# Kernel tuning notes

Hardware: AMD Instinct MI355X
Metric: run time of the kernel (lower is better)

Reference implementation:

```python
import jax, jax.numpy as jnp
import numpy as np

T = 3              # num_ntype (slots)
NH = 64            # num_hidden == num_classes
HEADS = (4, 4, 1)
NUM_ETYPES = 5
EDGE_DIM = 64
N_NODES = 20000
NEG_SLOPE = 0.2
ALPHA = 0.05       # residual-attention blend
EPS = 1e-12


def _l2_by_slot(x):
    # l2_norm with l2BySlot='True': normalize each ntype slot independently
    n = x.shape[0]
    xs = x.reshape(n, T, -1)
    nrm = jnp.linalg.norm(xs, axis=2, keepdims=True)
    return (xs / jnp.maximum(nrm, EPS)).reshape(n, -1)


def _edge_softmax(logits, dst, n):
    # softmax over incoming edges of each destination node
    m = jax.lax.stop_gradient(jax.ops.segment_max(logits, dst, num_segments=n))
    e = jnp.exp(logits - m[dst])
    s = jax.ops.segment_sum(e, dst, num_segments=n)
    return e / s[dst]


def _conv(x, src, dst, etype, W, al, ar, ee_tab, We, ae, res_attn, act):
    # slotGATConv: x [N,T,C], W [T,C,H*O], al/ar [H,T*O], ee_tab [R,De], We [De,H*De], ae [H,De]
    n = x.shape[0]
    H = al.shape[0]
    proj = jnp.einsum('ntc,tcd->ntd', x, W)                     # [N,T,H*O]
    O = proj.shape[-1] // H
    feat = proj.reshape(n, T, H, O).transpose(0, 2, 1, 3).reshape(n, H, T * O)
    el = jnp.einsum('nhd,hd->nh', feat, al)
    er = jnp.einsum('nhd,hd->nh', feat, ar)
    De = ee_tab.shape[1]
    ep = (ee_tab[etype] @ We).reshape(-1, H, De)                # [E,H,De]
    ee = jnp.einsum('ehd,hd->eh', ep, ae)                       # [E,H]
    logit = jax.nn.leaky_relu(el[src] + er[dst] + ee, NEG_SLOPE)
    a = _edge_softmax(logit, dst, n)                            # [E,H]
    if res_attn is not None:
        a = a * (1.0 - ALPHA) + res_attn * ALPHA
    out = jax.ops.segment_sum(feat[src] * a[:, :, None], dst, num_segments=n)  # [N,H,T*O]
    if act:
        out = jax.nn.elu(out)
    return out, a


def _forward(feat0, feat1, feat2, w_in0, b_in0, w_in1, b_in1, w_in2, b_in2,
             l0_W, l0_al, l0_ar, l0_ee, l0_we, l0_ae,
             l1_W, l1_al, l1_ar, l1_ee, l1_we, l1_ae,
             l2_W, l2_al, l2_ar, l2_ee, l2_we, l2_ae,
             dm_W, e_feat, src, dst, left, right, mid):
    feats = [feat0, feat1, feat2]
    lins = [(w_in0, b_in0), (w_in1, b_in1), (w_in2, b_in2)]
    blocks = []
    for t, (f, (w, b)) in enumerate(zip(feats, lins)):
        ft = f @ w + b                                          # [n_t, NH]
        pad = jnp.zeros((f.shape[0], T * NH), ft.dtype)
        blocks.append(pad.at[:, t * NH:(t + 1) * NH].set(ft))   # slot zero-padding
    h = jnp.concatenate(blocks, 0)                              # [N, T*NH]
    emb = [_l2_by_slot(h)]                                      # aggregator='None' -> identity
    x = h.reshape(-1, T, NH)
    out0, a0 = _conv(x, src, dst, e_feat, l0_W, l0_al, l0_ar, l0_ee, l0_we, l0_ae, None, True)
    emb.append(_l2_by_slot(out0.mean(1)))
    x = out0.reshape(-1, HEADS[0], T, NH).transpose(0, 2, 1, 3).reshape(-1, T, HEADS[0] * NH)
    out1, a1 = _conv(x, src, dst, e_feat, l1_W, l1_al, l1_ar, l1_ee, l1_we, l1_ae, a0, True)
    emb.append(_l2_by_slot(out1.mean(1)))
    x = out1.reshape(-1, HEADS[1], T, NH).transpose(0, 2, 1, 3).reshape(-1, T, HEADS[1] * NH)
    out2, _ = _conv(x, src, dst, e_feat, l2_W, l2_al, l2_ar, l2_ee, l2_we, l2_ae, a1, False)
    emb.append(_l2_by_slot(out2.mean(1)))
    # aggregator='None' + inProcessEmb='True': concat per-slot along feature dim
    embs = [e.reshape(-1, T, NH) for e in emb]
    o = jnp.concatenate(embs, 2).reshape(-1, T * NH * len(embs))  # [N, 768]
    le, re = o[left], o[right]
    scores = jnp.zeros(left.shape[0], o.dtype)
    for r in range(NUM_ETYPES):                                 # DistMult per relation
        s = ((le @ dm_W[r]) * re).sum(1)
        scores = jnp.where(mid == r, s, scores)
    return jax.nn.sigmoid(scores)


def setup_inputs() -> dict:
    key = jax.random.key(0)
    ks = iter(jax.random.split(key, 64))
    def nrm(shape, std):
        return jax.random.normal(next(ks), shape, jnp.float32) * std
    counts = [8000, 6000, 6000]
    in_dims = [256, 128, 64]
    inp = {}
    for t in range(T):
        inp[f'feat{t}'] = jax.random.normal(next(ks), (counts[t], in_dims[t]), jnp.float32)
        inp[f'w_in{t}'] = nrm((in_dims[t], NH), 0.1)
        inp[f'b_in{t}'] = nrm((NH,), 0.1)
    Cs = [NH, HEADS[0] * NH, HEADS[1] * NH]
    for l in range(3):
        H = HEADS[l]
        inp[f'l{l}_W'] = nrm((T, Cs[l], H * NH), 0.1)
        inp[f'l{l}_al'] = nrm((H, T * NH), 0.1)
        inp[f'l{l}_ar'] = nrm((H, T * NH), 0.1)
        inp[f'l{l}_ee'] = nrm((NUM_ETYPES, EDGE_DIM), 0.1)
        inp[f'l{l}_we'] = nrm((EDGE_DIM, H * EDGE_DIM), 0.1)
        inp[f'l{l}_ae'] = nrm((H, EDGE_DIM), 0.1)
    D = T * NH * 4
    inp['dm_W'] = nrm((NUM_ETYPES, D, D), 0.05)
    E, L = 200000, 10000
    inp['e_feat'] = jax.random.randint(next(ks), (E,), 0, NUM_ETYPES)
    inp['src'] = jax.random.randint(next(ks), (E,), 0, N_NODES)
    inp['dst'] = jax.random.randint(next(ks), (E,), 0, N_NODES)
    inp['left'] = jax.random.randint(next(ks), (L,), 0, N_NODES)
    inp['right'] = jax.random.randint(next(ks), (L,), 0, N_NODES)
    inp['mid'] = jax.random.randint(next(ks), (L,), 0, NUM_ETYPES)
    return inp


def reference(feat0, feat1, feat2, w_in0, b_in0, w_in1, b_in1, w_in2, b_in2,
              l0_W, l0_al, l0_ar, l0_ee, l0_we, l0_ae,
              l1_W, l1_al, l1_ar, l1_ee, l1_we, l1_ae,
              l2_W, l2_al, l2_ar, l2_ee, l2_we, l2_ae,
              dm_W, e_feat, src, dst, left, right, mid):
    return _forward(feat0, feat1, feat2, w_in0, b_in0, w_in1, b_in1, w_in2, b_in2,
                    l0_W, l0_al, l0_ar, l0_ee, l0_we, l0_ae,
                    l1_W, l1_al, l1_ar, l1_ee, l1_we, l1_ae,
                    l2_W, l2_al, l2_ar, l2_ee, l2_we, l2_ae,
                    dm_W, e_feat, src, dst, left, right, mid)
```

## Files before the change

### kernel.cpp

```cpp
#include <hip/hip_runtime.h>
#include <math.h>

#define N_NODES 20000
#define NPAD    20096
#define N_EDGES 200000
#define N_PAIRS 10000
#define PAIR_PAD 10368
#define DM_TILES 162
#define NBLK    79

typedef __attribute__((ext_vector_type(8))) short s16x8;
typedef __attribute__((ext_vector_type(4))) float f32x4;

__device__ inline float wave_max(float v){
  for (int o = 32; o > 0; o >>= 1) v = fmaxf(v, __shfl_xor(v, o));
  return v;
}
__device__ inline float wave_sum(float v){
  for (int o = 32; o > 0; o >>= 1) v += __shfl_xor(v, o);
  return v;
}
__device__ inline float half_max(float v){
  for (int o = 16; o > 0; o >>= 1) v = fmaxf(v, __shfl_xor(v, o));
  return v;
}
__device__ inline float half_sum(float v){
  for (int o = 16; o > 0; o >>= 1) v += __shfl_xor(v, o);
  return v;
}
__device__ inline short f2bf(float x){
  union { float f; unsigned u; } v; v.f = x;
  unsigned r = (v.u + 0x7FFFu + ((v.u >> 16) & 1u)) >> 16;
  return (short)r;
}
__device__ inline float bf2f(short s){
  union { unsigned u; float f; } v; v.u = ((unsigned)(unsigned short)s) << 16;
  return v.f;
}
__device__ inline int ntype(int s){ return (s < 8000) ? 0 : ((s < 14000) ? 1 : 2); }
__device__ inline float elu1(float x){ return (x > 0.f) ? x : expm1f(x); }

#define OS(i, c) ((i) * 100 + (c))

__global__ void build_h(const float* __restrict__ f0, const float* __restrict__ w0, const float* __restrict__ b0,
                        const float* __restrict__ f1, const float* __restrict__ w1, const float* __restrict__ b1,
                        const float* __restrict__ f2, const float* __restrict__ w2, const float* __restrict__ b2,
                        short* __restrict__ Xb0, short* __restrict__ o_b,
                        int* __restrict__ cnt3, int* __restrict__ cnt5, int* __restrict__ pos5,
                        float* __restrict__ score, int* __restrict__ pairs,
                        float* __restrict__ eall, short* __restrict__ Xb12,
                        short* __restrict__ featb){
  const int blk = blockIdx.x, lane = threadIdx.x;
  const int gid = blk * 64 + lane;
  if (gid < 80000) cnt3[gid] = 0;
  if (gid < 5){ cnt5[gid * 16] = 0; pos5[gid * 16] = 0; }
  if (gid < 10016) score[gid] = 0.f;
  if (gid < PAIR_PAD) pairs[gid] = -1;
  for (int i = gid; i < 480000; i += 160000) eall[i] = 0.f;
  s16x8 z = {};
  if (gid < 4608){
    int t = (gid * 16) / 24576, off = (gid * 16) % 24576;
    short* p = Xb12 + ((size_t)(t * NPAD + N_NODES)) * 256 + off;
    *(s16x8*)p = z; *(s16x8*)(p + 8) = z;
  }
  if (gid < 1152){
    int t = (gid * 16) / 6144, off = (gid * 16) % 6144;
    short* p = Xb0 + ((size_t)(t * NPAD + N_NODES)) * 64 + off;
    *(s16x8*)p = z; *(s16x8*)(p + 8) = z;
  }
  int t, C, nbase; const float *f, *w, *b;
  if (blk < 1000)       { t = 0; nbase = 0;     C = 256; f = f0; w = w0; b = b0; }
  else if (blk < 1750)  { t = 1; nbase = 8000;  C = 128; f = f1; w = w1; b = b1; }
  else                  { t = 2; nbase = 14000; C = 64;  f = f2; w = w2; b = b2; }
  const int n0 = blk * 8;
  const int n0l = n0 - nbase;
  __shared__ float xs[8 * 256];
  const float* fr = f + (size_t)n0l * C;
  for (int i = lane; i < 8 * C; i += 64) xs[i] = fr[i];
  __syncthreads();
  float acc[8];
#pragma unroll
  for (int j = 0; j < 8; j++) acc[j] = b[lane];
  for (int c = 0; c < C; c++){
    float wv = w[c * 64 + lane];
#pragma unroll
    for (int j = 0; j < 8; j++) acc[j] += xs[j * C + c] * wv;
  }
  for (int j = 0; j < 8; j++){
    int n = n0 + j;
    {
      int h = lane >> 4, si = (lane >> 3) & 1, j8 = lane & 7;
      int s0 = (t == 0) ? 1 : 0;
      int s1 = (t == 2) ? 1 : 2;
      int toff = si ? s1 : s0;
      *(s16x8*)(featb + ((size_t)n * 4 + h) * 192 + toff * 64 + j8 * 8) = z;
    }
    for (int tt = 0; tt < 3; tt++)
      Xb0[((size_t)(tt * NPAD) + n) * 64 + lane] = f2bf((tt == t) ? acc[j] : 0.f);
    float ss = wave_sum(acc[j] * acc[j]);
    float sc = 1.f / fmaxf(sqrtf(ss), 1e-12f);
    for (int tt = 0; tt < 3; tt++)
      o_b[(size_t)n * 768 + tt * 256 + lane] = f2bf((tt == t) ? acc[j] * sc : 0.f);
  }
}

__global__ void count_prep_k(const int* __restrict__ dst, const int* __restrict__ srcv,
                             int* __restrict__ cnt3,
                             const int* __restrict__ mid, int* __restrict__ cnt5,
                             const float* __restrict__ lW0, const float* __restrict__ lW1,
                             const float* __restrict__ lW2, const float* __restrict__ dmW,
                             short* __restrict__ Wt0, short* __restrict__ Wt1,
                             short* __restrict__ Wt2, short* __restrict__ Mt,
                             const float* __restrict__ ee0, const float* __restrict__ we0, const float* __restrict__ ae0,
                             const float* __restrict__ ee1, const float* __restrict__ we1, const float* __restrict__ ae1,
                             const float* __restrict__ ee2, const float* __restrict__ we2, const float* __restrict__ ae2,
                             float* __restrict__ ee5f){
  if (blockIdx.x < 782){
    int e = blockIdx.x * 256 + threadIdx.x;
    int lane = threadIdx.x & 63;
    if (e < N_EDGES){
      int tt = ntype(srcv[e]);
      atomicAdd(&cnt3[dst[e] * 4 + tt], 1);
    }
    int r_mine = (e < N_PAIRS) ? mid[e] : -1;
#pragma unroll
    for (int r = 0; r < 5; r++){
      unsigned long long mask = __ballot(r_mine == r);
      if (mask){
        int leader = __ffsll((long long)mask) - 1;
        if (lane == leader) atomicAdd(&cnt5[r * 16], __popcll(mask));
      }
    }
    return;
  }
  int lin = blockIdx.x - 782;
  int z = lin / 576;
  int rem = lin % 576;
  int by = rem / 24, bx = rem % 24;
  if (z == 10){
    int r = bx, L = by;
    if (r >= 5 || L >= 3) return;
    int H = (L == 2) ? 1 : 4;
    const float* eetab = (L == 0) ? ee0 : ((L == 1) ? ee1 : ee2);
    const float* We    = (L == 0) ? we0 : ((L == 1) ? we1 : we2);
    const float* ae    = (L == 0) ? ae0 : ((L == 1) ? ae1 : ae2);
    int h = threadIdx.x >> 6, lane = threadIdx.x & 63;
    if (h >= H) return;
    float v = 0.f;
    for (int k = 0; k < 64; k++) v += eetab[r * 64 + k] * We[k * H * 64 + h * 64 + lane];
    v *= ae[h * 64 + lane];
    v = wave_sum(v);
    if (lane == 0) ee5f[L * 32 + r * H + h] = v;
    return;
  }
  const float* s; short* d; int R, Cc, r0, c0;
  if (z < 5){
    s = dmW + (size_t)z * 589824; d = Mt + (size_t)z * 589824;
    R = 768; Cc = 768; r0 = bx * 32; c0 = by * 32;
  } else if (z < 8){
    if (bx >= 8 || by >= 8) return;
    int t = z - 5;
    s = lW1 + (size_t)t * 65536; d = Wt1 + (size_t)t * 65536;
    R = 256; Cc = 256; r0 = bx * 32; c0 = by * 32;
  } else if (z == 8){
    if (bx >= 6 || by >= 8) return;
    int t = bx >> 1;
    s = lW0 + (size_t)t * 16384; d = Wt0 + (size_t)t * 16384;
    R = 64; Cc = 256; r0 = (bx & 1) * 32; c0 = by * 32;
  } else {
    if (bx >= 8 || by >= 6) return;
    int t = by >> 1;
    s = lW2 + (size_t)t * 16384; d = Wt2 + (size_t)t * 16384;
    R = 256; Cc = 64; r0 = bx * 32; c0 = (by & 1) * 32;
  }
  __shared__ float tile[32][33];
  int tx = threadIdx.x & 31, ty = threadIdx.x >> 5;
  for (int i = 0; i < 32; i += 8){
    int r = r0 + ty + i;
    tile[ty + i][tx] = (r < R && c0 + tx < Cc) ? s[(size_t)r * Cc + c0 + tx] : 0.f;
  }
  __syncthreads();
  for (int i = 0; i < 32; i += 8){
    int c = c0 + ty + i;
    if (c < Cc && r0 + tx < R)
      d[(size_t)c * R + r0 + tx] = f2bf(tile[tx][ty + i]);
  }
}

__global__ void scan1_k(const int* __restrict__ cnt3, int* __restrict__ loc, int* __restrict__ bsum){
  __shared__ int s[256];
  int tid = threadIdx.x;
  int idx = blockIdx.x * 256 + tid;
  int v = (idx < N_NODES) ? (cnt3[idx * 4] + cnt3[idx * 4 + 1] + cnt3[idx * 4 + 2]) : 0;
  s[tid] = v;
  __syncthreads();
  for (int o = 1; o < 256; o <<= 1){
    int u = (tid >= o) ? s[tid - o] : 0;
    __syncthreads();
    s[tid] += u;
    __syncthreads();
  }
  if (idx < N_NODES) loc[idx] = s[tid] - v;
  if (tid == 255) bsum[blockIdx.x] = s[255];
}

__global__ void scan2_k(const int* __restrict__ bsum, int* __restrict__ bofs,
                        const int* __restrict__ cnt5, int* __restrict__ off5){
  __shared__ int s[128];
  int tid = threadIdx.x;
  int v = (tid < NBLK) ? bsum[tid] : 0;
  s[tid] = v;
  __syncthreads();
  for (int o = 1; o < 128; o <<= 1){
    int u = (tid >= o) ? s[tid - o] : 0;
    __syncthreads();
    s[tid] += u;
    __syncthreads();
  }
  if (tid < NBLK) bofs[tid] = s[tid] - v;
  if (tid == 0){
    int r0 = 0;
    for (int r = 0; r < 5; r++){ off5[r] = r0; r0 += ((cnt5[r * 16] + 63) >> 6) << 6; }
  }
}

__global__ void scan3_k(const int* __restrict__ loc, const int* __restrict__ bofs,
                        int* __restrict__ coff, int* __restrict__ cpos,
                        const int* __restrict__ cnt3){
  int idx = blockIdx.x * 256 + threadIdx.x;
  if (idx < N_NODES){
    int v = loc[idx] + bofs[blockIdx.x];
    coff[idx] = v;
    int c0 = cnt3[idx * 4], c1 = cnt3[idx * 4 + 1];
    cpos[idx * 4]     = v;
    cpos[idx * 4 + 1] = v + c0;
    cpos[idx * 4 + 2] = v + c0 + c1;
  }
  if (idx == 0) coff[N_NODES] = N_EDGES;
}

__global__ void scatter_k(const int* __restrict__ dst, const int* __restrict__ srcv,
                          const int* __restrict__ efeat, int* __restrict__ cpos,
                          int* __restrict__ src_sorted, int* __restrict__ et_sorted,
                          const int* __restrict__ mid, const int* __restrict__ off5,
                          int* __restrict__ pos5, int* __restrict__ pairs){
  int e = blockIdx.x * 256 + threadIdx.x;
  int lane = threadIdx.x & 63;
  if (e < N_EDGES){
    int s = srcv[e];
    int tt = ntype(s);
    int p = atomicAdd(&cpos[dst[e] * 4 + tt], 1);
    src_sorted[p] = s;
    et_sorted[p] = efeat[e];
  }
  int r_mine = (e < N_PAIRS) ? mid[e] : -1;
#pragma unroll
  for (int r = 0; r < 5; r++){
    unsigned long long mask = __ballot(r_mine == r);
    if (mask){
      int cnt = __popcll(mask);
      int leader = __ffsll((long long)mask) - 1;
      int base = 0;
      if (lane == leader) base = atomicAdd(&pos5[r * 16], cnt);
      base = __shfl(base, leader);
      if (r_mine == r){
        int rank = __popcll(mask & ((1ull << lane) - 1ull));
        pairs[off5[r] + base + rank] = e;
      }
    }
  }
}

template<int C, int NO, int TYPED>
__global__ void mfma_proj(const short* __restrict__ Xb, const short* __restrict__ Wt,
                          short* __restrict__ featb, const float* __restrict__ al,
                          const float* __restrict__ ar, float* __restrict__ elf,
                          float* __restrict__ erf){
  constexpr int H = NO / 64;
  const int ct = blockIdx.y;
  const int t  = blockIdx.z;
  int tile = blockIdx.x;
  if (TYPED){
    const int lo[3] = {0, 62, 109};
    const int hi[3] = {63, 110, 157};
    tile += lo[t];
    if (tile >= hi[t]) return;
  }
  const int n0 = tile * 128;
  const int tid = threadIdx.x;
  const int w = tid >> 6, lane = tid & 63;
  const int quad = lane >> 4, ln = lane & 15;
  __shared__ __attribute__((aligned(16))) short A_s[128 * 32];
  __shared__ __attribute__((aligned(16))) short B_s[64 * 32];
  const short* Xt  = Xb + (size_t)t * NPAD * C;
  const short* Wtt = Wt + ((size_t)t * NO + ct * 64) * C;
  f32x4 acc[2][4] = {};
  for (int kk = 0; kk < C; kk += 32){
    {
      int row = tid >> 1, half = tid & 1;
      const s16x8* g = (const s16x8*)(Xt + (size_t)(n0 + row) * C + kk + half * 16);
      s16x8 v0 = g[0], v1 = g[1];
      *(s16x8*)(A_s + row * 32 + half * 16) = v0;
      *(s16x8*)(A_s + row * 32 + half * 16 + 8) = v1;
    }
    {
      int row = tid >> 2, chunk = tid & 3;
      s16x8 v = *(const s16x8*)(Wtt + (size_t)row * C + kk + chunk * 8);
      *(s16x8*)(B_s + row * 32 + chunk * 8) = v;
    }
    __syncthreads();
    s16x8 af0 = *(s16x8*)(A_s + (w * 32 + ln) * 32 + quad * 8);
    s16x8 af1 = *(s16x8*)(A_s + (w * 32 + 16 + ln) * 32 + quad * 8);
    s16x8 bf[4];
#pragma unroll
    for (int b = 0; b < 4; b++) bf[b] = *(s16x8*)(B_s + (b * 16 + ln) * 32 + quad * 8);
#pragma unroll
    for (int b = 0; b < 4; b++){
      acc[0][b] = __builtin_amdgcn_mfma_f32_16x16x32_bf16(af0, bf[b], acc[0][b], 0, 0, 0);
      acc[1][b] = __builtin_amdgcn_mfma_f32_16x16x32_bf16(af1, bf[b], acc[1][b], 0, 0, 0);
    }
    __syncthreads();
  }
#pragma unroll
  for (int ar_ = 0; ar_ < 2; ar_++){
#pragma unroll
    for (int i = 0; i < 4; i++){
      int n = n0 + w * 32 + ar_ * 16 + quad * 4 + i;
      if (n >= N_NODES) continue;
#pragma unroll
      for (int b = 0; b < 4; b++){
        int jj = b * 16 + ln;
        featb[((size_t)n * H + ct) * 192 + t * 64 + jj] = f2bf(acc[ar_][b][i]);
      }
    }
  }
  float alv[4], arv[4];
#pragma unroll
  for (int b = 0; b < 4; b++){
    alv[b] = al[ct * 192 + t * 64 + b * 16 + ln];
    arv[b] = ar[ct * 192 + t * 64 + b * 16 + ln];
  }
#pragma unroll
  for (int ar_ = 0; ar_ < 2; ar_++){
#pragma unroll
    for (int i = 0; i < 4; i++){
      float pe = 0.f, pr = 0.f;
#pragma unroll
      for (int b = 0; b < 4; b++){
        pe += acc[ar_][b][i] * alv[b];
        pr += acc[ar_][b][i] * arv[b];
      }
#pragma unroll
      for (int o = 1; o < 16; o <<= 1){
        pe += __shfl_xor(pe, o);
        pr += __shfl_xor(pr, o);
      }
      int n = n0 + w * 32 + ar_ * 16 + quad * 4 + i;
      if (ln == 0 && n < N_NODES){
        atomicAdd(&elf[n * H + ct], pe);
        atomicAdd(&erf[n * H + ct], pr);
      }
    }
  }
}

template<int H, int MODE, int ACT, int TYPED>
__global__ __launch_bounds__(256) void gat_fused(
    const int* __restrict__ csr_off, const int* __restrict__ src_sorted,
    const int* __restrict__ et_sorted,
    const float* __restrict__ el, const float* __restrict__ er, const float* __restrict__ ee5,
    const float* __restrict__ aprev, float* __restrict__ aout,
    const short* __restrict__ featb, short* __restrict__ outb,
    short* __restrict__ o_b, const int* __restrict__ cnt3, int kslice){
  const int wid = threadIdx.x >> 6, lane = threadIdx.x & 63;
  const int half = lane >> 5, hl = lane & 31;
  const int l32 = half << 5;
  const int n0 = blockIdx.x * 8 + wid * 2;
  const int nme = n0 + half;
  __shared__ float a_s[4][64][H];
  __shared__ int   src_s[4][64];
  __shared__ float out_s[4][2][800];
  const char* fb = (const char*)featb;

  const int offm = csr_off[nme];
  const int cntm = csr_off[nme + 1] - offm;
  const int cnto = __shfl_xor(cntm, 32);
  const bool paired = (cntm <= 32) && (cnto <= 32);

  if (paired){
    float ern[H];
    if constexpr (H == 4){
      f32x4 ev = *(const f32x4*)(er + nme * 4);
#pragma unroll
      for (int h = 0; h < 4; h++) ern[h] = ev[h];
    } else ern[0] = er[nme];
    const int p = offm + hl;
    const bool valid = hl < cntm;
    int sidx = 0, r = 0;
    if (valid){ sidx = src_sorted[p]; r = et_sorted[p]; }
    int s0 = __shfl(sidx, l32);
    src_s[wid][lane] = (valid ? sidx : s0) * (H * 384);
    float lg[H];
#pragma unroll
    for (int h = 0; h < H; h++) lg[h] = -1e30f;
    if (valid){
      if constexpr (H == 4){
        f32x4 elv = *(const f32x4*)(el + sidx * 4);
        f32x4 eev = *(const f32x4*)(ee5 + r * 4);
#pragma unroll
        for (int h = 0; h < 4; h++){
          float v = elv[h] + ern[h] + eev[h];
          lg[h] = (v >= 0.f) ? v : 0.2f * v;
        }
      } else {
        float v = el[sidx] + ern[0] + ee5[r];
        lg[0] = (v >= 0.f) ? v : 0.2f * v;
      }
    }
    float ap[4] = {};
    if (MODE > 0 && valid){
      f32x4 av4 = *(const f32x4*)(aprev + (size_t)p * 4);
#pragma unroll
      for (int q = 0; q < 4; q++) ap[q] = av4[q];
    }
    float av[H];
#pragma unroll
    for (int h = 0; h < H; h++){
      float mh = half_max(lg[h]);
      float ex = valid ? __expf(lg[h] - mh) : 0.f;
      float sh = half_sum(ex);
      float a = ex / sh;
      if (MODE == 1) a = 0.95f * a + 0.05f * ap[h];
      if (MODE == 2) a = 0.95f * a + 0.0125f * (ap[0] + ap[1] + ap[2] + ap[3]);
      av[h] = a;
      a_s[wid][lane][h] = valid ? a : 0.f;
    }
    if constexpr (MODE != 2){
      if (valid){
        f32x4 o = {av[0], av[1], av[2], av[3]};
        *(f32x4*)(aout + (size_t)p * 4) = o;
      }
    }

    if constexpr (TYPED && H == 4){
      const int hh = hl >> 3, j8 = hl & 7;
      float acc[3][8] = {};
      const int b1 = cnt3[nme * 4], b2 = b1 + cnt3[nme * 4 + 1];
      const int rb[4] = {0, b1, b2, cntm};
#pragma unroll
      for (int t = 0; t < 3; t++){
        const int sub = hh * 384 + t * 128 + j8 * 16;
        for (int b = rb[t]; b < rb[t + 1]; b += 2){
          int e0 = l32 + b;
          bool v1 = (b + 1) < rb[t + 1];
          int e1 = v1 ? e0 + 1 : e0;
          float a0 = a_s[wid][e0][hh];
          float a1 = v1 ? a_s[wid][e1][hh] : 0.f;
          int so0 = src_s[wid][e0], so1 = src_s[wid][e1];
          s16x8 f0 = *(const s16x8*)(fb + so0 + sub);
          s16x8 f1 = *(const s16x8*)(fb + so1 + sub);
#pragma unroll
          for (int i = 0; i < 8; i++) acc[t][i] += a0 * bf2f(f0[i]) + a1 * bf2f(f1[i]);
        }
      }
#pragma unroll
      for (int t = 0; t < 3; t++){
#pragma unroll
        for (int i = 0; i < 8; i++){
          float v = acc[t][i];
          if (ACT) v = elu1(v);
          out_s[wid][half][OS(i, hh * 24 + t * 8 + j8)] = v;
        }
      }
    } else if constexpr (H == 4){
      const int p0 = hl, p1 = hl + 32, p2 = hl + 64;
      const int h0 = p0 / 24, h1 = p1 / 24, h2 = p2 / 24;
      float acc0[8] = {}, acc1[8] = {}, acc2[8] = {};
      const int cnt2 = (cntm + 1) & ~1;
      for (int b = 0; b < cnt2; b += 2){
        int e0 = l32 + b, e1 = l32 + b + 1;
        int so0 = src_s[wid][e0], so1 = src_s[wid][e1];
        float a00 = a_s[wid][e0][h0], a01 = a_s[wid][e0][h1], a02 = a_s[wid][e0][h2];
        float a10 = a_s[wid][e1][h0], a11 = a_s[wid][e1][h1], a12 = a_s[wid][e1][h2];
        s16x8 f00 = *(const s16x8*)(fb + so0 + p0 * 16);
        s16x8 f01 = *(const s16x8*)(fb + so0 + p1 * 16);
        s16x8 f02 = *(const s16x8*)(fb + so0 + p2 * 16);
        s16x8 f10 = *(const s16x8*)(fb + so1 + p0 * 16);
        s16x8 f11 = *(const s16x8*)(fb + so1 + p1 * 16);
        s16x8 f12 = *(const s16x8*)(fb + so1 + p2 * 16);
#pragma unroll
        for (int i = 0; i < 8; i++){
          acc0[i] += a00 * bf2f(f00[i]) + a10 * bf2f(f10[i]);
          acc1[i] += a01 * bf2f(f01[i]) + a11 * bf2f(f11[i]);
          acc2[i] += a02 * bf2f(f02[i]) + a12 * bf2f(f12[i]);
        }
      }
#pragma unroll
      for (int i = 0; i < 8; i++){
        float v0 = acc0[i], v1 = acc1[i], v2 = acc2[i];
        if (ACT){ v0 = elu1(v0); v1 = elu1(v1); v2 = elu1(v2); }
        out_s[wid][half][OS(i, p0)] = v0;
        out_s[wid][half][OS(i, p1)] = v1;
        out_s[wid][half][OS(i, p2)] = v2;
      }
    } else {
      const int e4 = hl >> 3, cb = hl & 7;
      float acc[3][8] = {};
      for (int b = 0; b < cntm; b += 4){
        int e = l32 + b + e4;
        float a = a_s[wid][e][0];
        int so = src_s[wid][e];
#pragma unroll
        for (int c = 0; c < 3; c++){
          s16x8 fv = *(const s16x8*)(fb + so + (cb * 3 + c) * 16);
#pragma unroll
          for (int i = 0; i < 8; i++) acc[c][i] += a * bf2f(fv[i]);
        }
      }
#pragma unroll
      for (int c = 0; c < 3; c++){
#pragma unroll
        for (int i = 0; i < 8; i++){
          float v = acc[c][i];
          v += __shfl_xor(v, 8); v += __shfl_xor(v, 16);
          if (ACT) v = elu1(v);
          if (e4 == 0) out_s[wid][half][OS(i, cb * 3 + c)] = v;
        }
      }
    }
  } else {
    for (int k = 0; k < 2; k++){
      const int n = n0 + k;
      const int off = csr_off[n];
      const int cnt = csr_off[n + 1] - off;
      float* osk = out_s[wid][k];
      float ern[H];
#pragma unroll
      for (int h = 0; h < H; h++) ern[h] = er[n * H + h];
      if (cnt <= 64){
        int p = off + lane;
        int sidx = 0, r = 0;
        if (lane < cnt){ sidx = src_sorted[p]; r = et_sorted[p]; }
        int src0 = __shfl(sidx, 0);
        src_s[wid][lane] = ((lane < cnt) ? sidx : src0) * (H * 384);
        float lg[H];
#pragma unroll
        for (int h = 0; h < H; h++) lg[h] = -1e30f;
        if (lane < cnt){
#pragma unroll
          for (int h = 0; h < H; h++){
            float v = el[sidx * H + h] + ern[h] + ee5[r * H + h];
            lg[h] = (v >= 0.f) ? v : 0.2f * v;
          }
        }
        float ap[4] = {};
        if (MODE > 0 && lane < cnt){
#pragma unroll
          for (int q = 0; q < 4; q++) ap[q] = aprev[(size_t)p * 4 + q];
        }
        float av[H];
#pragma unroll
        for (int h = 0; h < H; h++){
          float mh = wave_max(lg[h]);
          float ex = (lane < cnt) ? __expf(lg[h] - mh) : 0.f;
          float sh = wave_sum(ex);
          float a = ex / sh;
          if (MODE == 1) a = 0.95f * a + 0.05f * ap[h];
          if (MODE == 2) a = 0.95f * a + 0.0125f * (ap[0] + ap[1] + ap[2] + ap[3]);
          av[h] = a;
          a_s[wid][lane][h] = (lane < cnt) ? a : 0.f;
        }
        if constexpr (MODE != 2){
          if (lane < cnt){
            f32x4 o = {av[0], av[1], av[2], av[3]};
            *(f32x4*)(aout + (size_t)p * 4) = o;
          }
        }
        if constexpr (H == 4){
          const int p0 = lane;
          const int p1 = (lane < 32) ? lane + 64 : lane - 32;
          const int p2 = lane + 32;
          const int hA = p0 / 24, hB = p1 / 24, hC = p2 / 24;
          const int eo2 = lane >> 5;
          float acc0[8] = {}, acc1[8] = {}, acc2[8] = {};
          const int cnt4 = (cnt + 3) & ~3;
          for (int b = 0; b < cnt4; b += 4){
            int eB0 = b + eo2, eB1 = b + 2 + eo2;
            int oA0 = src_s[wid][b],     oB0 = src_s[wid][eB0], oC0 = src_s[wid][b + 1];
            int oA1 = src_s[wid][b + 2], oB1 = src_s[wid][eB1], oC1 = src_s[wid][b + 3];
            float aA0 = a_s[wid][b][hA],     aB0 = a_s[wid][eB0][hB], aC0 = a_s[wid][b + 1][hC];
            float aA1 = a_s[wid][b + 2][hA], aB1 = a_s[wid][eB1][hB], aC1 = a_s[wid][b + 3][hC];
            s16x8 fA0 = *(const s16x8*)(fb + oA0 + p0 * 16);
            s16x8 fB0 = *(const s16x8*)(fb + oB0 + p1 * 16);
            s16x8 fC0 = *(const s16x8*)(fb + oC0 + p2 * 16);
            s16x8 fA1 = *(const s16x8*)(fb + oA1 + p0 * 16);
            s16x8 fB1 = *(const s16x8*)(fb + oB1 + p1 * 16);
            s16x8 fC1 = *(const s16x8*)(fb + oC1 + p2 * 16);
#pragma unroll
            for (int i = 0; i < 8; i++){
              acc0[i] += aA0 * bf2f(fA0[i]) + aA1 * bf2f(fA1[i]);
              acc1[i] += aB0 * bf2f(fB0[i]) + aB1 * bf2f(fB1[i]);
              acc2[i] += aC0 * bf2f(fC0[i]) + aC1 * bf2f(fC1[i]);
            }
          }
#pragma unroll
          for (int i = 0; i < 8; i++){
            float v1 = (lane < 32) ? acc2[i] : acc1[i];
            float r1 = __shfl_xor(v1, 32);
            float v0 = acc0[i] + r1;
            if (ACT) v0 = elu1(v0);
            osk[OS(i, p0)] = v0;
            float r2 = __shfl_xor(acc2[i], 32);
            if (lane < 32){
              float vv = acc1[i] + r2;
              if (ACT) vv = elu1(vv);
              osk[OS(i, p1)] = vv;
            }
          }
        } else {
          const int eo = lane & 7, cb = lane >> 3;
          float acc[3][8] = {};
          for (int b = 0; b < cnt; b += 8){
            int e = b + eo;
            float a = a_s[wid][e][0];
            int so = src_s[wid][e];
#pragma unroll
            for (int c = 0; c < 3; c++){
              s16x8 fv = *(const s16x8*)(fb + so + (cb * 3 + c) * 16);
#pragma unroll
              for (int i = 0; i < 8; i++) acc[c][i] += a * bf2f(fv[i]);
            }
          }
#pragma unroll
          for (int c = 0; c < 3; c++){
#pragma unroll
            for (int i = 0; i < 8; i++){
              float v = acc[c][i];
              v += __shfl_xor(v, 1); v += __shfl_xor(v, 2); v += __shfl_xor(v, 4);
              if (ACT) v = elu1(v);
              if (eo == 0) osk[OS(i, cb * 3 + c)] = v;
            }
          }
        }
      } else {
        constexpr int NC = H * 192 / 8;
        const int c0 = lane, h0 = (c0 / 24) % H;
        const int c1 = lane + 64, h1 = (c1 / 24) % H;
        const bool act0 = (c0 < NC);
        const bool act1 = (H == 4) && (lane < 32);
        float acc0[8] = {}, acc1[8] = {};
        float mh[H], sh[H];
#pragma unroll
        for (int h = 0; h < H; h++){ mh[h] = -1e30f; sh[h] = 0.f; }
        for (int b = lane; b < cnt; b += 64){
          int pp = off + b; int s = src_sorted[pp]; int r = et_sorted[pp];
#pragma unroll
          for (int h = 0; h < H; h++){
            float v = el[s * H + h] + ern[h] + ee5[r * H + h];
            v = (v >= 0.f) ? v : 0.2f * v;
            mh[h] = fmaxf(mh[h], v);
          }
        }
#pragma unroll
        for (int h = 0; h < H; h++) mh[h] = wave_max(mh[h]);
        for (int b = lane; b < cnt; b += 64){
          int pp = off + b; int s = src_sorted[pp]; int r = et_sorted[pp];
#pragma unroll
          for (int h = 0; h < H; h++){
            float v = el[s * H + h] + ern[h] + ee5[r * H + h];
            v = (v >= 0.f) ? v : 0.2f * v;
            sh[h] += __expf(v - mh[h]);
          }
        }
#pragma unroll
        for (int h = 0; h < H; h++) sh[h] = wave_sum(sh[h]);
        if (MODE != 2){
          for (int b = lane; b < cnt; b += 64){
            int pp = off + b; int s = src_sorted[pp]; int r = et_sorted[pp];
            float ap[4] = {};
            if (MODE > 0){
#pragma unroll
              for (int q = 0; q < 4; q++) ap[q] = aprev[(size_t)pp * 4 + q];
            }
            float av[4] = {};
#pragma unroll
            for (int h = 0; h < H; h++){
              float v = el[s * H + h] + ern[h] + ee5[r * H + h];
              v = (v >= 0.f) ? v : 0.2f * v;
              float a = __expf(v - mh[h]) / sh[h];
              if (MODE == 1) a = 0.95f * a + 0.05f * ap[h];
              av[h] = a;
            }
            f32x4 o = {av[0], av[1], av[2], av[3]};
            *(f32x4*)(aout + (size_t)pp * 4) = o;
          }
        }
        for (int b = 0; b < cnt; b++){
          int pp = off + b; int s = src_sorted[pp]; int r = et_sorted[pp];
          const short* row = featb + (size_t)s * (H * 192);
          float apm[4] = {};
          if (MODE > 0){
#pragma unroll
            for (int q = 0; q < 4; q++) apm[q] = aprev[(size_t)pp * 4 + q];
          }
          if (act0){
            float v = el[s * H + h0] + ern[h0] + ee5[r * H + h0];
            v = (v >= 0.f) ? v : 0.2f * v;
            float a = __expf(v - mh[h0]) / sh[h0];
            if (MODE == 1) a = 0.95f * a + 0.05f * apm[h0];
            if (MODE == 2) a = 0.95f * a + 0.0125f * (apm[0] + apm[1] + apm[2] + apm[3]);
            s16x8 vv = *(const s16x8*)(row + c0 * 8);
#pragma unroll
            for (int i = 0; i < 8; i++) acc0[i] += a * bf2f(vv[i]);
          }
          if (act1){
            float v = el[s * H + h1] + ern[h1] + ee5[r * H + h1];
            v = (v >= 0.f) ? v : 0.2f * v;
            float a = __expf(v - mh[h1]) / sh[h1];
            if (MODE == 1) a = 0.95f * a + 0.05f * apm[h1];
            s16x8 vv = *(const s16x8*)(row + c1 * 8);
#pragma unroll
            for (int i = 0; i < 8; i++) acc1[i] += a * bf2f(vv[i]);
          }
        }
        if (act0){
#pragma unroll
          for (int i = 0; i < 8; i++) osk[OS(i, c0)] = ACT ? elu1(acc0[i]) : acc0[i];
        }
        if (act1){
#pragma unroll
          for (int i = 0; i < 8; i++) osk[OS(i, c1)] = ACT ? elu1(acc1[i]) : acc1[i];
        }
      }
    }
  }

  const float* os = out_s[wid][half];
  if (outb){
    if constexpr (H == 4){
#pragma unroll
      for (int cc = 0; cc < 3; cc++){
        int c = hl + cc * 32;
        int dd = c * 8, h = dd / 192, rr = dd % 192, t = rr / 64, j = rr % 64;
        s16x8 o;
#pragma unroll
        for (int i = 0; i < 8; i++) o[i] = f2bf(os[OS(i, c)]);
        *(s16x8*)(outb + ((size_t)(t * NPAD) + nme) * 256 + h * 64 + j) = o;
      }
    } else {
      if (hl < 24){
        int c = hl;
        int t = (c * 8) / 64, j = (c * 8) % 64;
        s16x8 o;
#pragma unroll
        for (int i = 0; i < 8; i++) o[i] = f2bf(os[OS(i, c)]);
        *(s16x8*)(outb + ((size_t)(t * NPAD) + nme) * 256 + j) = o;
      }
    }
  }
  const int cb8 = hl >> 3, ib = hl & 7;
  for (int t = 0; t < 3; t++){
    float va, vb;
    if constexpr (H == 4){
      va = 0.25f * (os[OS(ib, t * 8 + cb8)] + os[OS(ib, 24 + t * 8 + cb8)] +
                    os[OS(ib, 48 + t * 8 + cb8)] + os[OS(ib, 72 + t * 8 + cb8)]);
      vb = 0.25f * (os[OS(ib, t * 8 + cb8 + 4)] + os[OS(ib, 24 + t * 8 + cb8 + 4)] +
                    os[OS(ib, 48 + t * 8 + cb8 + 4)] + os[OS(ib, 72 + t * 8 + cb8 + 4)]);
    } else {
      va = os[OS(ib, t * 8 + cb8)];
      vb = os[OS(ib, t * 8 + cb8 + 4)];
    }
    float ss = half_sum(va * va + vb * vb);
    float sc = 1.f / fmaxf(sqrtf(ss), 1e-12f);
    short* ob = o_b + (size_t)nme * 768 + t * 256 + kslice * 64;
    ob[hl] = f2bf(va * sc);
    ob[hl + 32] = f2bf(vb * sc);
  }
}

__global__ void distmult_mfma(const short* __restrict__ o_b, const short* __restrict__ Mt,
                              const int* __restrict__ pairs, const int* __restrict__ left,
                              const int* __restrict__ right, const int* __restrict__ mid,
                              float* __restrict__ score){
  const int pt = blockIdx.x, ct = blockIdx.y;
  const int tid = threadIdx.x;
  const int w = tid >> 6, lane = tid & 63;
  const int quad = lane >> 4, ln = lane & 15;
  __shared__ __attribute__((aligned(16))) short smem[8192];
  short* A_s = smem;
  short* B_s = smem + 2048;
  __shared__ int pid_s[64];
  __shared__ int lbase[64];
  if (tid < 64){
    int p = pairs[pt * 64 + tid];
    pid_s[tid] = p;
    lbase[tid] = (p >= 0) ? left[p] * 768 : 0;
  }
  __syncthreads();
  int p0 = pid_s[0];
  if (p0 < 0) return;
  const int r = mid[p0];
  const short* Mr = Mt + (size_t)r * 768 * 768;
  f32x4 acc[8] = {};
  for (int kk = 0; kk < 768; kk += 32){
    {
      int row = tid >> 2, chunk = tid & 3;
      s16x8 v = *(const s16x8*)(o_b + (size_t)lbase[row] + kk + chunk * 8);
      *(s16x8*)(A_s + row * 32 + chunk * 8) = v;
    }
    {
      int row = tid >> 1, half = tid & 1;
      const s16x8* g = (const s16x8*)(Mr + (size_t)(ct * 128 + row) * 768 + kk + half * 16);
      s16x8 v0 = g[0], v1 = g[1];
      *(s16x8*)(B_s + row * 32 + half * 16) = v0;
      *(s16x8*)(B_s + row * 32 + half * 16 + 8) = v1;
    }
    __syncthreads();
    s16x8 af = *(s16x8*)(A_s + (w * 16 + ln) * 32 + quad * 8);
#pragma unroll
    for (int b = 0; b < 8; b++){
      s16x8 bf = *(s16x8*)(B_s + (b * 16 + ln) * 32 + quad * 8);
      acc[b] = __builtin_amdgcn_mfma_f32_16x16x32_bf16(af, bf, acc[b], 0, 0, 0);
    }
    __syncthreads();
  }
  short* RE_s = smem;
  {
    int row = tid >> 2, quarter = tid & 3;
    int p = pid_s[row];
    s16x8 v0 = {}, v1 = {}, v2 = {}, v3 = {};
    if (p >= 0){
      const s16x8* g = (const s16x8*)(o_b + (size_t)right[p] * 768 + ct * 128 + quarter * 32);
      v0 = g[0]; v1 = g[1]; v2 = g[2]; v3 = g[3];
    }
    __syncthreads();
    short* dst = RE_s + row * 128 + quarter * 32;
    *(s16x8*)(dst)      = v0;
    *(s16x8*)(dst + 8)  = v1;
    *(s16x8*)(dst + 16) = v2;
    *(s16x8*)(dst + 24) = v3;
  }
  __syncthreads();
#pragma unroll
  for (int i = 0; i < 4; i++){
    int row = w * 16 + quad * 4 + i;
    float s = 0.f;
#pragma unroll
    for (int b = 0; b < 8; b++)
      s += acc[b][i] * bf2f(RE_s[row * 128 + b * 16 + ln]);
    s += __shfl_xor(s, 1); s += __shfl_xor(s, 2);
    s += __shfl_xor(s, 4); s += __shfl_xor(s, 8);
    if (ln == 0){
      int p = pid_s[row];
      if (p >= 0) atomicAdd(&score[p], s);
    }
  }
}

__global__ void sigmoid_k(const float* __restrict__ score, float* __restrict__ out){
  int i = blockIdx.x * 256 + threadIdx.x;
  if (i < N_PAIRS) out[i] = 1.f / (1.f + __expf(-score[i]));
}

extern "C" void kernel_launch(void* const* d_in, const int* in_sizes, int n_in,
                              void* d_out, int out_size, void* d_ws, size_t ws_size,
                              hipStream_t stream){
  const float* f0 = (const float*)d_in[0];
  const float* w0 = (const float*)d_in[1];
  const float* b0 = (const float*)d_in[2];
  const float* f1 = (const float*)d_in[3];
  const float* w1 = (const float*)d_in[4];
  const float* b1 = (const float*)d_in[5];
  const float* f2 = (const float*)d_in[6];
  const float* w2_ = (const float*)d_in[7];
  const float* b2 = (const float*)d_in[8];
  const float* lW[3]  = {(const float*)d_in[9],  (const float*)d_in[15], (const float*)d_in[21]};
  const float* lal[3] = {(const float*)d_in[10], (const float*)d_in[16], (const float*)d_in[22]};
  const float* lar[3] = {(const float*)d_in[11], (const float*)d_in[17], (const float*)d_in[23]};
  const float* lee[3] = {(const float*)d_in[12], (const float*)d_in[18], (const float*)d_in[24]};
  const float* lwe[3] = {(const float*)d_in[13], (const float*)d_in[19], (const float*)d_in[25]};
  const float* lae[3] = {(const float*)d_in[14], (const float*)d_in[20], (const float*)d_in[26]};
  const float* dmW = (const float*)d_in[27];
  const int* efeat = (const int*)d_in[28];
  const int* srcv  = (const int*)d_in[29];
  const int* dstv  = (const int*)d_in[30];
  const int* left  = (const int*)d_in[31];
  const int* right = (const int*)d_in[32];
  const int* midv  = (const int*)d_in[33];
  float* out = (float*)d_out;

  short* feat_b = (short*)d_ws;
  float* aA     = (float*)(feat_b + 15360000);
  float* aB     = aA + 800000;
  float* eall   = aB + 800000;
  float* ee5f   = eall + 480000;
  float* score  = ee5f + 96;
  int* cnt3     = (int*)(score + 10016);
  int* csr_off  = cnt3 + 80000;
  int* csr_pos  = csr_off + 20004;
  int* loc      = csr_pos + 80000;
  int* bsum     = loc + 20000;
  int* bofs     = bsum + 128;
  int* src_sorted = bofs + 128;
  int* et_sorted  = src_sorted + 200000;
  int* cnt5     = et_sorted + 200000;
  int* off5     = cnt5 + 80;
  int* pos5     = off5 + 8;
  int* pairs    = pos5 + 80;
  short* o_b    = (short*)(pairs + PAIR_PAD);
  short* Xb0    = o_b + 15360000;
  short* Xb12   = Xb0 + 3858432;
  short* Wt0    = Xb12 + 15433728;
  short* Wt1    = Wt0 + 49152;
  short* Wt2    = Wt1 + 196608;
  short* Mt     = Wt2 + 49152;
  float* elf0 = eall, *erf0 = eall + 80000;
  float* elf1 = eall + 160000, *erf1 = eall + 240000;
  float* elf2 = eall + 320000, *erf2 = eall + 400000;

  build_h<<<2500, 64, 0, stream>>>(f0, w0, b0, f1, w1, b1, f2, w2_, b2, Xb0, o_b,
                                   cnt3, cnt5, pos5, score, pairs, eall, Xb12, feat_b);
  count_prep_k<<<782 + 6336, 256, 0, stream>>>(dstv, srcv, cnt3, midv, cnt5,
                                               lW[0], lW[1], lW[2], dmW, Wt0, Wt1, Wt2, Mt,
                                               lee[0], lwe[0], lae[0], lee[1], lwe[1], lae[1],
                                               lee[2], lwe[2], lae[2], ee5f);
  scan1_k<<<NBLK, 256, 0, stream>>>(cnt3, loc, bsum);
  scan2_k<<<1, 128, 0, stream>>>(bsum, bofs, cnt5, off5);
  scan3_k<<<NBLK, 256, 0, stream>>>(loc, bofs, csr_off, csr_pos, cnt3);
  scatter_k<<<782, 256, 0, stream>>>(dstv, srcv, efeat, csr_pos, src_sorted, et_sorted,
                                     midv, off5, pos5, pairs);

  { dim3 g(64, 4, 3);
    mfma_proj<64, 256, 1><<<g, 256, 0, stream>>>(Xb0, Wt0, feat_b, lal[0], lar[0], elf0, erf0); }
  gat_fused<4, 0, 1, 1><<<2500, 256, 0, stream>>>(csr_off, src_sorted, et_sorted, elf0, erf0, ee5f,
                                                  nullptr, aA, feat_b, Xb12, o_b, cnt3, 1);

  { dim3 g(NPAD / 128, 4, 3);
    mfma_proj<256, 256, 0><<<g, 256, 0, stream>>>(Xb12, Wt1, feat_b, lal[1], lar[1], elf1, erf1); }
  gat_fused<4, 1, 1, 0><<<2500, 256, 0, stream>>>(csr_off, src_sorted, et_sorted, elf1, erf1, ee5f + 32,
                                                  aA, aB, feat_b, Xb12, o_b, cnt3, 2);

  { dim3 g(NPAD / 128, 1, 3);
    mfma_proj<256, 64, 0><<<g, 256, 0, stream>>>(Xb12, Wt2, feat_b, lal[2], lar[2], elf2, erf2); }
  gat_fused<1, 2, 0, 0><<<2500, 256, 0, stream>>>(csr_off, src_sorted, et_sorted, elf2, erf2, ee5f + 64,
                                                  aB, nullptr, feat_b, nullptr, o_b, cnt3, 3);

  { dim3 g(DM_TILES, 6); distmult_mfma<<<g, 256, 0, stream>>>(o_b, Mt, pairs, left, right, midv, score); }
  sigmoid_k<<<40, 256, 0, stream>>>(score, out);
}
```

Baseline: 447.5 us.

## Compute all head column tiles per block in mfma_proj and pad LDS rows

Each projection block now computes all H output column tiles instead of one per blockIdx.y. This lets the A tile (node features) load once and be reused across heads, cutting redundant global reads of X by a factor of H. The LDS row stride is padded from 32 to 40 shorts to reduce bank conflicts. In exchange, accumulator register use grows (2*H*4 f32x4), which may lower occupancy, and the grid is 4x smaller, so there is less parallelism.

```diff
diff --git a/kernel.cpp b/kernel.cpp
--- a/kernel.cpp
+++ b/kernel.cpp
@@ -271,13 +271,13 @@
   }
 }
 
+#define LDA 40
 template<int C, int NO, int TYPED>
 __global__ void mfma_proj(const short* __restrict__ Xb, const short* __restrict__ Wt,
                           short* __restrict__ featb, const float* __restrict__ al,
                           const float* __restrict__ ar, float* __restrict__ elf,
                           float* __restrict__ erf){
   constexpr int H = NO / 64;
-  const int ct = blockIdx.y;
   const int t  = blockIdx.z;
   int tile = blockIdx.x;
   if (TYPED){
@@ -290,75 +290,83 @@
   const int tid = threadIdx.x;
   const int w = tid >> 6, lane = tid & 63;
   const int quad = lane >> 4, ln = lane & 15;
-  __shared__ __attribute__((aligned(16))) short A_s[128 * 32];
-  __shared__ __attribute__((aligned(16))) short B_s[64 * 32];
+  __shared__ __attribute__((aligned(16))) short A_s[128 * LDA];
+  __shared__ __attribute__((aligned(16))) short B_s[NO * LDA];
   const short* Xt  = Xb + (size_t)t * NPAD * C;
-  const short* Wtt = Wt + ((size_t)t * NO + ct * 64) * C;
-  f32x4 acc[2][4] = {};
+  const short* Wtt = Wt + (size_t)t * NO * C;
+  f32x4 acc[2][H][4] = {};
   for (int kk = 0; kk < C; kk += 32){
     {
-      int row = tid >> 1, half = tid & 1;
-      const s16x8* g = (const s16x8*)(Xt + (size_t)(n0 + row) * C + kk + half * 16);
+      int row = tid >> 1, hk = tid & 1;
+      const s16x8* g = (const s16x8*)(Xt + (size_t)(n0 + row) * C + kk + hk * 16);
       s16x8 v0 = g[0], v1 = g[1];
-      *(s16x8*)(A_s + row * 32 + half * 16) = v0;
-      *(s16x8*)(A_s + row * 32 + half * 16 + 8) = v1;
-    }
-    {
-      int row = tid >> 2, chunk = tid & 3;
+      *(s16x8*)(A_s + row * LDA + hk * 16) = v0;
+      *(s16x8*)(A_s + row * LDA + hk * 16 + 8) = v1;
+    }
+#pragma unroll
+    for (int rr = 0; rr < NO / 64; rr++){
+      int row = (tid >> 2) + rr * 64, chunk = tid & 3;
       s16x8 v = *(const s16x8*)(Wtt + (size_t)row * C + kk + chunk * 8);
-      *(s16x8*)(B_s + row * 32 + chunk * 8) = v;
+      *(s16x8*)(B_s + row * LDA + chunk * 8) = v;
     }
     __syncthreads();
-    s16x8 af0 = *(s16x8*)(A_s + (w * 32 + ln) * 32 + quad * 8);
-    s16x8 af1 = *(s16x8*)(A_s + (w * 32 + 16 + ln) * 32 + quad * 8);
-    s16x8 bf[4];
-#pragma unroll
-    for (int b = 0; b < 4; b++) bf[b] = *(s16x8*)(B_s + (b * 16 + ln) * 32 + quad * 8);
+    s16x8 af0 = *(s16x8*)(A_s + (w * 32 + ln) * LDA + quad * 8);
+    s16x8 af1 = *(s16x8*)(A_s + (w * 32 + 16 + ln) * LDA + quad * 8);
+#pragma unroll
+    for (int ct = 0; ct < H; ct++){
+#pragma unroll
+      for (int b = 0; b < 4; b++){
+        s16x8 bf = *(s16x8*)(B_s + (ct * 64 + b * 16 + ln) * LDA + quad * 8);
+        acc[0][ct][b] = __builtin_amdgcn_mfma_f32_16x16x32_bf16(af0, bf, acc[0][ct][b], 0, 0, 0);
+        acc[1][ct][b] = __builtin_amdgcn_mfma_f32_16x16x32_bf16(af1, bf, acc[1][ct][b], 0, 0, 0);
+      }
+    }
+    __syncthreads();
+  }
+#pragma unroll
+  for (int ct = 0; ct < H; ct++){
+#pragma unroll
+    for (int ar_ = 0; ar_ < 2; ar_++){
+#pragma unroll
+      for (int i = 0; i < 4; i++){
+        int n = n0 + w * 32 + ar_ * 16 + quad * 4 + i;
+        if (n >= N_NODES) continue;
+#pragma unroll
+        for (int b = 0; b < 4; b++){
+          int jj = b * 16 + ln;
+          featb[((size_t)n * H + ct) * 192 + t * 64 + jj] = f2bf(acc[ar_][ct][b][i]);
+        }
+      }
+    }
+  }
+#pragma unroll
+  for (int ct = 0; ct < H; ct++){
+    float alv[4], arv[4];
 #pragma unroll
     for (int b = 0; b < 4; b++){
-      acc[0][b] = __builtin_amdgcn_mfma_f32_16x16x32_bf16(af0, bf[b], acc[0][b], 0, 0, 0);
-      acc[1][b] = __builtin_amdgcn_mfma_f32_16x16x32_bf16(af1, bf[b], acc[1][b], 0, 0, 0);
-    }
-    __syncthreads();
-  }
-#pragma unroll
-  for (int ar_ = 0; ar_ < 2; ar_++){
-#pragma unroll
-    for (int i = 0; i < 4; i++){
-      int n = n0 + w * 32 + ar_ * 16 + quad * 4 + i;
-      if (n >= N_NODES) continue;
-#pragma unroll
-      for (int b = 0; b < 4; b++){
-        int jj = b * 16 + ln;
-        featb[((size_t)n * H + ct) * 192 + t * 64 + jj] = f2bf(acc[ar_][b][i]);
-      }
-    }
-  }
-  float alv[4], arv[4];
-#pragma unroll
-  for (int b = 0; b < 4; b++){
-    alv[b] = al[ct * 192 + t * 64 + b * 16 + ln];
-    arv[b] = ar[ct * 192 + t * 64 + b * 16 + ln];
-  }
-#pragma unroll
-  for (int ar_ = 0; ar_ < 2; ar_++){
-#pragma unroll
-    for (int i = 0; i < 4; i++){
-      float pe = 0.f, pr = 0.f;
-#pragma unroll
-      for (int b = 0; b < 4; b++){
-        pe += acc[ar_][b][i] * alv[b];
-        pr += acc[ar_][b][i] * arv[b];
-      }
-#pragma unroll
-      for (int o = 1; o < 16; o <<= 1){
-        pe += __shfl_xor(pe, o);
-        pr += __shfl_xor(pr, o);
-      }
-      int n = n0 + w * 32 + ar_ * 16 + quad * 4 + i;
-      if (ln == 0 && n < N_NODES){
-        atomicAdd(&elf[n * H + ct], pe);
-        atomicAdd(&erf[n * H + ct], pr);
+      alv[b] = al[ct * 192 + t * 64 + b * 16 + ln];
+      arv[b] = ar[ct * 192 + t * 64 + b * 16 + ln];
+    }
+#pragma unroll
+    for (int ar_ = 0; ar_ < 2; ar_++){
+#pragma unroll
+      for (int i = 0; i < 4; i++){
+        float pe = 0.f, pr = 0.f;
+#pragma unroll
+        for (int b = 0; b < 4; b++){
+          pe += acc[ar_][ct][b][i] * alv[b];
+          pr += acc[ar_][ct][b][i] * arv[b];
+        }
+#pragma unroll
+        for (int o = 1; o < 16; o <<= 1){
+          pe += __shfl_xor(pe, o);
+          pr += __shfl_xor(pr, o);
+        }
+        int n = n0 + w * 32 + ar_ * 16 + quad * 4 + i;
+        if (ln == 0 && n < N_NODES){
+          atomicAdd(&elf[n * H + ct], pe);
+          atomicAdd(&erf[n * H + ct], pr);
+        }
       }
     }
   }
@@ -930,12 +938,12 @@
   scatter_k<<<782, 256, 0, stream>>>(dstv, srcv, efeat, csr_pos, src_sorted, et_sorted,
                                      midv, off5, pos5, pairs);
 
-  { dim3 g(64, 4, 3);
+  { dim3 g(64, 1, 3);
     mfma_proj<64, 256, 1><<<g, 256, 0, stream>>>(Xb0, Wt0, feat_b, lal[0], lar[0], elf0, erf0); }
   gat_fused<4, 0, 1, 1><<<2500, 256, 0, stream>>>(csr_off, src_sorted, et_sorted, elf0, erf0, ee5f,
                                                   nullptr, aA, feat_b, Xb12, o_b, cnt3, 1);
 
-  { dim3 g(NPAD / 128, 4, 3);
+  { dim3 g(NPAD / 128, 1, 3);
     mfma_proj<256, 256, 0><<<g, 256, 0, stream>>>(Xb12, Wt1, feat_b, lal[1], lar[1], elf1, erf1); }
   gat_fused<4, 1, 1, 0><<<2500, 256, 0, stream>>>(csr_off, src_sorted, et_sorted, elf1, erf1, ee5f + 32,
                                                   aA, aB, feat_b, Xb12, o_b, cnt3, 2);
```

After: 506.9 us. 1.13x slower.
